# Performance work log

Hardware: AMD Instinct MI355X
Metric: run time of the kernel (lower is better)

The kernel has to match this reference:

```python
import jax, jax.numpy as jnp
import numpy as np

NUM_CODES = 8192
EMBED_DIM = 256
N_TOKENS = 65536
COMMITMENT_COST = 0.25


def setup_inputs() -> dict:
    key = jax.random.key(0)
    k1, k2 = jax.random.split(key)
    inputs = jax.random.normal(k1, (N_TOKENS, EMBED_DIM), dtype=jnp.float32)
    # torch init: uniform(-1/num_codes, 1/num_codes); use normal-scale equivalent via uniform
    weight = jax.random.uniform(k2, (NUM_CODES, EMBED_DIM), dtype=jnp.float32,
                                minval=-1.0 / NUM_CODES, maxval=1.0 / NUM_CODES)
    return {"inputs": inputs, "weight": weight}


def reference(inputs, weight):
    inputs_sq = jnp.sum(inputs * inputs, axis=1, keepdims=True)      # (N, 1)
    embed_sq = jnp.sum(weight * weight, axis=1)                      # (K,)
    distances = inputs_sq + embed_sq - 2.0 * (inputs @ weight.T)     # (N, K)
    indices = jnp.argmin(distances, axis=1)                          # (N,)
    quantized = jnp.take(weight, indices, axis=0)                    # (N, D)

    codebook_loss = jnp.mean((quantized - jax.lax.stop_gradient(inputs)) ** 2)
    commit_loss = jnp.mean((inputs - jax.lax.stop_gradient(quantized)) ** 2)
    vq_loss = codebook_loss + COMMITMENT_COST * commit_loss

    # straight-through estimator
    quantized_st = inputs + jax.lax.stop_gradient(quantized - inputs)
    return quantized_st, indices, vq_loss, codebook_loss, commit_loss
```

## Files before the change

### kernel.cpp

```cpp
#include <hip/hip_runtime.h>

#define N_TOK  65536
#define N_CODE 8192
#define DIM    256

typedef _Float16 f16;
typedef _Float16 f16x8 __attribute__((ext_vector_type(8)));
typedef float    f32x4 __attribute__((ext_vector_type(4)));

__global__ __launch_bounds__(256) void rowsq_kernel(const float* __restrict__ src,
                                                    float* __restrict__ dst, int nrows) {
    int row  = blockIdx.x * 4 + (threadIdx.x >> 6);
    int lane = threadIdx.x & 63;
    if (row >= nrows) return;
    float4 v = ((const float4*)(src + (size_t)row * DIM))[lane];
    float s = v.x * v.x + v.y * v.y + v.z * v.z + v.w * v.w;
#pragma unroll
    for (int off = 32; off; off >>= 1) s += __shfl_down(s, off, 64);
    if (lane == 0) dst[row] = s;
}

__global__ __launch_bounds__(256) void splitw_kernel(const float* __restrict__ W,
                                                     f16* __restrict__ W1,
                                                     f16* __restrict__ W2) {
    int f = blockIdx.x * 256 + threadIdx.x;
    float4 v = ((const float4*)W)[f];
    union { f16 h[4]; uint2 u; } p1, p2;
    float e[4] = {v.x, v.y, v.z, v.w};
#pragma unroll
    for (int i = 0; i < 4; ++i) {
        float ws = e[i] * 16384.0f;
        f16 w1 = (f16)ws;
        float r = (ws - (float)w1) * 2048.0f;
        p1.h[i] = w1; p2.h[i] = (f16)r;
    }
    ((uint2*)W1)[f] = p1.u;
    ((uint2*)W2)[f] = p2.u;
}

__global__ __launch_bounds__(256, 2) void argmin_mfma5(
    const float* __restrict__ X, const f16* __restrict__ W1, const f16* __restrict__ W2,
    const float* __restrict__ sxq, const float* __restrict__ esq,
    int* __restrict__ out_idx) {

    __shared__ char wbuf[65536];

    const int tid  = threadIdx.x;
    const int lane = tid & 63;
    const int wv   = tid >> 6;
    const int cl   = lane & 15;
    const int q    = lane >> 4;
    const int wavetok0 = blockIdx.x * 128 + wv * 32;

    f16x8 a1[2][8], a2[2][8];
#pragma unroll
    for (int mt = 0; mt < 2; ++mt)
#pragma unroll
        for (int s = 0; s < 8; ++s) {
            const float* p = X + (size_t)(wavetok0 + mt * 16 + cl) * DIM + s * 32 + q * 8;
            float4 v0 = ((const float4*)p)[0];
            float4 v1 = ((const float4*)p)[1];
            float e[8] = {v0.x, v0.y, v0.z, v0.w, v1.x, v1.y, v1.z, v1.w};
#pragma unroll
            for (int j = 0; j < 8; ++j) {
                f16 h = (f16)e[j];
                float r = (e[j] - (float)h) * 2048.0f;
                a1[mt][s][j] = h;
                a2[mt][s][j] = (f16)r;
            }
        }

    float sxr[8];
#pragma unroll
    for (int mt = 0; mt < 2; ++mt)
#pragma unroll
        for (int r = 0; r < 4; ++r)
            sxr[mt * 4 + r] = sxq[wavetok0 + mt * 16 + q * 4 + r];

    float bestd[8];
    int   besti[8];
#pragma unroll
    for (int i = 0; i < 8; ++i) { bestd[i] = 3.4e38f; besti[i] = 0x7fffffff; }

    auto stage = [&](int ct2, int sel) {
#pragma unroll
        for (int t = 0; t < 8; ++t) {
            int fi = wv * 8 + t;
            int L  = fi >> 4;
            int nt = (fi >> 3) & 1;
            int s  = fi & 7;
            const f16* gsrc = (L ? W2 : W1)
                + (size_t)(ct2 * 32 + nt * 16 + (lane & 15)) * DIM
                + s * 32 + (lane >> 4) * 8;
            char* ldst = wbuf + sel * 32768 + L * 16384 + nt * 8192 + s * 1024;
            __builtin_amdgcn_global_load_lds(
                (const __attribute__((address_space(1))) unsigned int*)gsrc,
                (__attribute__((address_space(3))) unsigned int*)ldst, 16, 0, 0);
        }
    };

    stage(0, 0);
    __syncthreads();

    for (int ct = 0; ct < N_CODE / 32; ++ct) {
        if (ct + 1 < N_CODE / 32) stage(ct + 1, (ct + 1) & 1);

        float se0 = esq[ct * 32 + cl];
        float se1 = esq[ct * 32 + 16 + cl];

        f32x4 mainA[2][2], cross[2][2];
#pragma unroll
        for (int mt = 0; mt < 2; ++mt)
#pragma unroll
            for (int nt = 0; nt < 2; ++nt) {
                mainA[mt][nt] = (f32x4){0.f, 0.f, 0.f, 0.f};
                cross[mt][nt] = (f32x4){0.f, 0.f, 0.f, 0.f};
            }

        const char* base = wbuf + (ct & 1) * 32768 + (lane << 4);
#pragma unroll
        for (int s = 0; s < 8; ++s) {
            f16x8 b1[2], b2[2];
#pragma unroll
            for (int nt = 0; nt < 2; ++nt) {
                b1[nt] = *(const f16x8*)(base + nt * 8192 + s * 1024);
                b2[nt] = *(const f16x8*)(base + 16384 + nt * 8192 + s * 1024);
            }
            __builtin_amdgcn_s_setprio(1);
#pragma unroll
            for (int mt = 0; mt < 2; ++mt)
#pragma unroll
                for (int nt = 0; nt < 2; ++nt) {
                    mainA[mt][nt] = __builtin_amdgcn_mfma_f32_16x16x32_f16(a1[mt][s], b1[nt], mainA[mt][nt], 0, 0, 0);
                    cross[mt][nt] = __builtin_amdgcn_mfma_f32_16x16x32_f16(a2[mt][s], b1[nt], cross[mt][nt], 0, 0, 0);
                    cross[mt][nt] = __builtin_amdgcn_mfma_f32_16x16x32_f16(a1[mt][s], b2[nt], cross[mt][nt], 0, 0, 0);
                }
            __builtin_amdgcn_s_setprio(0);
        }

#pragma unroll
        for (int mt = 0; mt < 2; ++mt)
#pragma unroll
            for (int nt = 0; nt < 2; ++nt)
#pragma unroll
                for (int r = 0; r < 4; ++r) {
                    float mc = fmaf(cross[mt][nt][r], 4.8828125e-4f, mainA[mt][nt][r]);
                    float t1 = sxr[mt * 4 + r] + (nt ? se1 : se0);
                    float d  = fmaf(-1.220703125e-4f, mc, t1);
                    int slot = mt * 4 + r;
                    if (d < bestd[slot]) {
                        bestd[slot] = d;
                        besti[slot] = ct * 32 + nt * 16 + cl;
                    }
                }
        __syncthreads();
    }

#pragma unroll
    for (int slot = 0; slot < 8; ++slot) {
        float d = bestd[slot];
        int   i = besti[slot];
#pragma unroll
        for (int off = 1; off < 16; off <<= 1) {
            float od = __shfl_xor(d, off, 64);
            int   oi = __shfl_xor(i, off, 64);
            if (od < d || (od == d && oi < i)) { d = od; i = oi; }
        }
        if (cl == 0)
            out_idx[wavetok0 + (slot >> 2) * 16 + q * 4 + (slot & 3)] = i;
    }
}

__global__ __launch_bounds__(256) void finalize_kernel(
    const float* __restrict__ X, const float* __restrict__ W,
    const int* __restrict__ idx, float* __restrict__ outQ,
    float* __restrict__ outI, double* __restrict__ accum) {
    __shared__ double wsum[4];
    int wid  = threadIdx.x >> 6;
    int lane = threadIdx.x & 63;
    int token = blockIdx.x * 4 + wid;
    int id = idx[token];
    float4 x = ((const float4*)(X + (size_t)token * DIM))[lane];
    float4 qv = ((const float4*)(W + (size_t)id * DIM))[lane];
    float4 o;
    o.x = x.x + (qv.x - x.x);
    o.y = x.y + (qv.y - x.y);
    o.z = x.z + (qv.z - x.z);
    o.w = x.w + (qv.w - x.w);
    ((float4*)(outQ + (size_t)token * DIM))[lane] = o;
    float dx = x.x - qv.x, dy = x.y - qv.y, dz = x.z - qv.z, dw = x.w - qv.w;
    float s = dx * dx + dy * dy + dz * dz + dw * dw;
#pragma unroll
    for (int off = 32; off; off >>= 1) s += __shfl_down(s, off, 64);
    if (lane == 0) {
        outI[token] = (float)id;
        wsum[wid] = (double)s;
    }
    __syncthreads();
    if (threadIdx.x == 0) {
        double t = wsum[0] + wsum[1] + wsum[2] + wsum[3];
        atomicAdd(&accum[blockIdx.x & 127], t);
    }
}

__global__ void scalars_kernel(const double* __restrict__ accum, float* __restrict__ out) {
    double mse = 0.0;
    for (int i = 0; i < 128; ++i) mse += accum[i];
    mse /= (double)((size_t)N_TOK * DIM);
    float c = (float)mse;
    out[0] = c + 0.25f * c;
    out[1] = c;
    out[2] = c;
}

extern "C" void kernel_launch(void* const* d_in, const int* in_sizes, int n_in,
                              void* d_out, int out_size, void* d_ws, size_t ws_size,
                              hipStream_t stream) {
    const float* X = (const float*)d_in[0];
    const float* W = (const float*)d_in[1];

    float* outQ = (float*)d_out;
    float* outI = outQ + (size_t)N_TOK * DIM;
    float* outS = outI + N_TOK;

    char* ws = (char*)d_ws;
    double* accum = (double*)ws;
    float* esq = (float*)(ws + 4096);
    float* sxq = (float*)(ws + 4096 + 32768);
    int*   idx = (int*)(ws + 4096 + 32768 + 262144);
    f16*   W1  = (f16*)(ws + (1 << 20));
    f16*   W2  = (f16*)(ws + (1 << 20) + 4194304);

    hipMemsetAsync(accum, 0, 128 * sizeof(double), stream);
    splitw_kernel<<<N_CODE * DIM / 4 / 256, 256, 0, stream>>>(W, W1, W2);
    rowsq_kernel<<<N_CODE / 4, 256, 0, stream>>>(W, esq, N_CODE);
    rowsq_kernel<<<N_TOK / 4, 256, 0, stream>>>(X, sxq, N_TOK);
    argmin_mfma5<<<N_TOK / 128, 256, 0, stream>>>(X, W1, W2, sxq, esq, idx);
    finalize_kernel<<<N_TOK / 4, 256, 0, stream>>>(X, W, idx, outQ, outI, accum);
    scalars_kernel<<<1, 1, 0, stream>>>(accum, outS);
}
```

Baseline: 828.7 us.

## Pre-transpose split codebook into octet-major layout for coalesced LDS staging

```diff
diff --git a/kernel.cpp b/kernel.cpp
--- a/kernel.cpp
+++ b/kernel.cpp
@@ -20,26 +20,31 @@
     if (lane == 0) dst[row] = s;
 }
 
-__global__ __launch_bounds__(256) void splitw_kernel(const float* __restrict__ W,
-                                                     f16* __restrict__ W1,
-                                                     f16* __restrict__ W2) {
-    int f = blockIdx.x * 256 + threadIdx.x;
-    float4 v = ((const float4*)W)[f];
-    union { f16 h[4]; uint2 u; } p1, p2;
-    float e[4] = {v.x, v.y, v.z, v.w};
-#pragma unroll
-    for (int i = 0; i < 4; ++i) {
+__global__ __launch_bounds__(256) void splitw_t_kernel(const float* __restrict__ W,
+                                                       f16* __restrict__ W1t,
+                                                       f16* __restrict__ W2t) {
+    int g = blockIdx.x * 256 + threadIdx.x;
+    int o = g >> 13;
+    int c = g & 8191;
+    const float* p = W + (size_t)c * DIM + o * 8;
+    float4 v0 = ((const float4*)p)[0];
+    float4 v1 = ((const float4*)p)[1];
+    float e[8] = {v0.x, v0.y, v0.z, v0.w, v1.x, v1.y, v1.z, v1.w};
+    union { f16 h[8]; uint4 u; } p1, p2;
+#pragma unroll
+    for (int i = 0; i < 8; ++i) {
         float ws = e[i] * 16384.0f;
         f16 w1 = (f16)ws;
         float r = (ws - (float)w1) * 2048.0f;
         p1.h[i] = w1; p2.h[i] = (f16)r;
     }
-    ((uint2*)W1)[f] = p1.u;
-    ((uint2*)W2)[f] = p2.u;
-}
-
-__global__ __launch_bounds__(256, 2) void argmin_mfma5(
-    const float* __restrict__ X, const f16* __restrict__ W1, const f16* __restrict__ W2,
+    size_t byteoff = (size_t)o * 131072 + (size_t)c * 16;
+    *(uint4*)((char*)W1t + byteoff) = p1.u;
+    *(uint4*)((char*)W2t + byteoff) = p2.u;
+}
+
+__global__ __launch_bounds__(256, 2) void argmin_mfma8(
+    const float* __restrict__ X, const f16* __restrict__ W1t, const f16* __restrict__ W2t,
     const float* __restrict__ sxq, const float* __restrict__ esq,
     int* __restrict__ out_idx) {
 
@@ -50,6 +55,8 @@
     const int wv   = tid >> 6;
     const int cl   = lane & 15;
     const int q    = lane >> 4;
+    const int l5   = lane >> 5;
+    const int lane31 = lane & 31;
     const int wavetok0 = blockIdx.x * 128 + wv * 32;
 
     f16x8 a1[2][8], a2[2][8];
@@ -82,17 +89,19 @@
 #pragma unroll
     for (int i = 0; i < 8; ++i) { bestd[i] = 3.4e38f; besti[i] = 0x7fffffff; }
 
+    const int SL = l5 * 131072 + lane31 * 16;
+    const char* RB = wbuf + q * 512 + cl * 16;
+
     auto stage = [&](int ct2, int sel) {
+        const char* g1 = (const char*)W1t + ct2 * 512 + SL;
+        const char* g2 = (const char*)W2t + ct2 * 512 + SL;
 #pragma unroll
         for (int t = 0; t < 8; ++t) {
             int fi = wv * 8 + t;
             int L  = fi >> 4;
-            int nt = (fi >> 3) & 1;
-            int s  = fi & 7;
-            const f16* gsrc = (L ? W2 : W1)
-                + (size_t)(ct2 * 32 + nt * 16 + (lane & 15)) * DIM
-                + s * 32 + (lane >> 4) * 8;
-            char* ldst = wbuf + sel * 32768 + L * 16384 + nt * 8192 + s * 1024;
+            int op = fi & 15;
+            const char* gsrc = (L ? g2 : g1) + op * 262144;
+            char* ldst = wbuf + sel * 32768 + L * 16384 + op * 1024;
             __builtin_amdgcn_global_load_lds(
                 (const __attribute__((address_space(1))) unsigned int*)gsrc,
                 (__attribute__((address_space(3))) unsigned int*)ldst, 16, 0, 0);
@@ -117,15 +126,14 @@
                 cross[mt][nt] = (f32x4){0.f, 0.f, 0.f, 0.f};
             }
 
-        const char* base = wbuf + (ct & 1) * 32768 + (lane << 4);
+        const char* va = RB + ((ct & 1) << 15);
 #pragma unroll
         for (int s = 0; s < 8; ++s) {
             f16x8 b1[2], b2[2];
-#pragma unroll
-            for (int nt = 0; nt < 2; ++nt) {
-                b1[nt] = *(const f16x8*)(base + nt * 8192 + s * 1024);
-                b2[nt] = *(const f16x8*)(base + 16384 + nt * 8192 + s * 1024);
-            }
+            b1[0] = *(const f16x8*)(va + s * 2048);
+            b1[1] = *(const f16x8*)(va + s * 2048 + 256);
+            b2[0] = *(const f16x8*)(va + s * 2048 + 16384);
+            b2[1] = *(const f16x8*)(va + s * 2048 + 16640);
             __builtin_amdgcn_s_setprio(1);
 #pragma unroll
             for (int mt = 0; mt < 2; ++mt)
@@ -228,14 +236,14 @@
     float* esq = (float*)(ws + 4096);
     float* sxq = (float*)(ws + 4096 + 32768);
     int*   idx = (int*)(ws + 4096 + 32768 + 262144);
-    f16*   W1  = (f16*)(ws + (1 << 20));
-    f16*   W2  = (f16*)(ws + (1 << 20) + 4194304);
+    f16*   W1t = (f16*)(ws + (1 << 20));
+    f16*   W2t = (f16*)(ws + (1 << 20) + 4194304);
 
     hipMemsetAsync(accum, 0, 128 * sizeof(double), stream);
-    splitw_kernel<<<N_CODE * DIM / 4 / 256, 256, 0, stream>>>(W, W1, W2);
+    splitw_t_kernel<<<N_CODE * 32 / 256, 256, 0, stream>>>(W, W1t, W2t);
     rowsq_kernel<<<N_CODE / 4, 256, 0, stream>>>(W, esq, N_CODE);
     rowsq_kernel<<<N_TOK / 4, 256, 0, stream>>>(X, sxq, N_TOK);
-    argmin_mfma5<<<N_TOK / 128, 256, 0, stream>>>(X, W1, W2, sxq, esq, idx);
+    argmin_mfma8<<<N_TOK / 128, 256, 0, stream>>>(X, W1t, W2t, sxq, esq, idx);
     finalize_kernel<<<N_TOK / 4, 256, 0, stream>>>(X, W, idx, outQ, outI, accum);
     scalars_kernel<<<1, 1, 0, stream>>>(accum, outS);
 }
```

Result: faster. 745.1 us (-10.1%).
